# Optimization experiments

Measured on AMD Instinct MI355X. Metric: run time of the kernel, lower is better.

Reference implementation:

```python
import jax, jax.numpy as jnp
import numpy as np

WBITS = 4
ABITS = 8
OBITS = 8


def fwht(x):
    """Normalized fast Walsh-Hadamard transform along the last axis (n power of 2).
    Equivalent to matmul_hadU with had_K = I, K = 1 (n = 4096 = 2^12)."""
    shape = x.shape
    n = shape[-1]
    x = x.reshape(-1, n)
    h = 1
    while h < n:
        x = x.reshape(-1, n // (2 * h), 2, h)
        a, b = x[:, :, 0, :], x[:, :, 1, :]
        x = jnp.concatenate([a + b, a - b], axis=-1).reshape(-1, n)
        h *= 2
    inv_sqrt_n = jnp.asarray(1.0 / np.sqrt(n), x.dtype)
    return (x * inv_sqrt_n).reshape(shape)


def sym_fake_quant(t, bits, axis):
    """Symmetric min-max RTN fake quantization (per-channel for weights,
    per-token for activations)."""
    qmax = jnp.asarray(2.0 ** (bits - 1) - 1.0, t.dtype)
    scale = jnp.max(jnp.abs(t), axis=axis, keepdims=True) / qmax
    scale = jnp.maximum(scale, jnp.asarray(1e-8, t.dtype))
    q = jnp.clip(jnp.round(t / scale), -qmax, qmax)
    return q * scale


def setup_inputs() -> dict:
    key = jax.random.key(0)
    k1, k2, k3 = jax.random.split(key, 3)
    B, S, DIN, DOUT = 4, 2048, 4096, 4096
    return {
        "input": jax.random.normal(k1, (B, S, DIN), dtype=jnp.float32),
        "weight": jax.random.normal(k2, (DOUT, DIN), dtype=jnp.float32) * 0.02,
        "bias": jax.random.normal(k3, (DOUT,), dtype=jnp.float32) * 0.01,
    }


def reference(input, weight, bias):
    # online full Hadamard rotation of activations
    x = fwht(input)
    # activation quant (per-token, symmetric int8 fake-quant)
    x = sym_fake_quant(x, ABITS, axis=-1)
    # weight quant (per-output-channel, symmetric int4 fake-quant)
    w = sym_fake_quant(weight, WBITS, axis=-1)
    # F.linear: x @ w.T + b
    out = jnp.einsum("bsi,oi->bso", x, w) + bias
    # output quant (per-token, symmetric int8 fake-quant)
    out = sym_fake_quant(out, OBITS, axis=-1)
    return out
```

## Files before the change

### kernel.cpp

```cpp
#include <hip/hip_runtime.h>
#include <hip/hip_bf16.h>

#define DIN 4096
#define DOUT 4096
#define NROWS 8192

typedef int i32x4 __attribute__((ext_vector_type(4)));

__device__ __forceinline__ float block_absmax(float m, float* red) {
  #pragma unroll
  for (int off = 32; off > 0; off >>= 1)
    m = fmaxf(m, __shfl_down(m, off));
  const int tid = threadIdx.x;
  if ((tid & 63) == 0) red[tid >> 6] = m;
  __syncthreads();
  return fmaxf(fmaxf(red[0], red[1]), fmaxf(red[2], red[3]));
}

__global__ __launch_bounds__(256) void fwht_quant_kernel(
    const float* __restrict__ in, char* __restrict__ qx,
    float* __restrict__ sx) {
  __shared__ float lds[4352];
  __shared__ float red[4];
  const int tid = threadIdx.x;
  const size_t row = blockIdx.x;
  const int th = tid >> 4, tl = tid & 15;
  float v[16];

  const float4* src = (const float4*)(in + row * DIN);
  #pragma unroll
  for (int k = 0; k < 4; ++k) {
    float4 f = src[tid * 4 + k];
    v[4 * k + 0] = f.x; v[4 * k + 1] = f.y;
    v[4 * k + 2] = f.z; v[4 * k + 3] = f.w;
  }
  #pragma unroll
  for (int hb = 1; hb < 16; hb <<= 1)
    #pragma unroll
    for (int j = 0; j < 16; ++j)
      if (!(j & hb)) {
        float a0 = v[j], b0 = v[j | hb];
        v[j] = a0 + b0; v[j | hb] = a0 - b0;
      }
  #pragma unroll
  for (int j = 0; j < 16; ++j) lds[17 * tid + j] = v[j];
  __syncthreads();
  #pragma unroll
  for (int j = 0; j < 16; ++j) v[j] = lds[272 * th + 17 * j + tl];
  #pragma unroll
  for (int hb = 1; hb < 16; hb <<= 1)
    #pragma unroll
    for (int j = 0; j < 16; ++j)
      if (!(j & hb)) {
        float a0 = v[j], b0 = v[j | hb];
        v[j] = a0 + b0; v[j | hb] = a0 - b0;
      }
  #pragma unroll
  for (int j = 0; j < 16; ++j) lds[272 * th + 17 * j + tl] = v[j];
  __syncthreads();
  #pragma unroll
  for (int j = 0; j < 16; ++j) v[j] = lds[272 * j + 17 * th + tl];
  #pragma unroll
  for (int hb = 1; hb < 16; hb <<= 1)
    #pragma unroll
    for (int j = 0; j < 16; ++j)
      if (!(j & hb)) {
        float a0 = v[j], b0 = v[j | hb];
        v[j] = a0 + b0; v[j | hb] = a0 - b0;
      }
  float m = 0.0f;
  #pragma unroll
  for (int j = 0; j < 16; ++j) m = fmaxf(m, fabsf(v[j]));
  #pragma unroll
  for (int j = 0; j < 16; ++j) lds[272 * j + 17 * th + tl] = v[j];
  float mx = block_absmax(m, red) * 0.015625f;
  float scale = fmaxf(mx / 127.0f, 1e-8f);
  if (tid == 0) sx[row] = scale;
  const float rs = 1.0f / scale;
  char pk[16];
  #pragma unroll
  for (int j = 0; j < 16; ++j) {
    float q = fminf(fmaxf(rintf((lds[17 * tid + j] * 0.015625f) * rs), -127.f),
                    127.f);
    pk[j] = (char)q;
  }
  *(int4*)(qx + row * DIN + (size_t)tid * 16) = *(const int4*)pk;
}

__global__ __launch_bounds__(256) void wquant_kernel(
    const float* __restrict__ w, char* __restrict__ qw,
    float* __restrict__ sw) {
  __shared__ float buf[DIN];
  __shared__ float red[4];
  const int tid = threadIdx.x;
  const size_t row = blockIdx.x;
  const float4* src = (const float4*)(w + row * DIN);
  float4* b4 = (float4*)buf;
  float m = 0.0f;
  for (int i = tid; i < DIN / 4; i += 256) {
    float4 v = src[i];
    b4[i] = v;
    m = fmaxf(m, fmaxf(fmaxf(fabsf(v.x), fabsf(v.y)),
                       fmaxf(fabsf(v.z), fabsf(v.w))));
  }
  float mx = block_absmax(m, red);
  float scale = fmaxf(mx / 7.0f, 1e-8f);
  if (tid == 0) sw[row] = scale;
  char* dst = qw + row * DIN;
  const float rs = 1.0f / scale;
  for (int i0 = tid * 4; i0 < DIN; i0 += 1024) {
    char4 pk;
    float q0 = fminf(fmaxf(rintf(buf[i0 + 0] * rs), -7.f), 7.f);
    float q1 = fminf(fmaxf(rintf(buf[i0 + 1] * rs), -7.f), 7.f);
    float q2 = fminf(fmaxf(rintf(buf[i0 + 2] * rs), -7.f), 7.f);
    float q3 = fminf(fmaxf(rintf(buf[i0 + 3] * rs), -7.f), 7.f);
    pk.x = (char)q0; pk.y = (char)q1; pk.z = (char)q2; pk.w = (char)q3;
    *(char4*)(dst + i0) = pk;
  }
}

__global__ __launch_bounds__(512, 2) void gemm_kernel(
    const char* __restrict__ A,
    const char* __restrict__ Bt,
    const float* __restrict__ sx, const float* __restrict__ sw,
    const float* __restrict__ bias, float* __restrict__ out) {
  __shared__ char lds[131072];
  const int tid = threadIdx.x;
  const int lane = tid & 63;
  const int wid = tid >> 6;
  const int wr = wid >> 2;
  const int wc = wid & 3;
  int bid = blockIdx.x;
  int swz = (bid & 7) * 64 + (bid >> 3);
  const int tm = swz >> 4;
  const int tn = swz & 15;
  const size_t row0 = (size_t)tm * 256;
  const size_t col0 = (size_t)tn * 256;
  const int slot0 = (((lane >> 4) ^ (lane & 7)) << 4);

  i32x4 acc[4][2][4] = {};
  i32x4 fb[4][2];
  i32x4 fa[2][2];

#define STAGE(MAT, GROW0, KT, LBASE)                                          \
  {                                                                           \
    _Pragma("unroll")                                                         \
    for (int j = 0; j < 2; ++j) {                                             \
      int chunk = j * 8 + wid;                                                \
      int rr = chunk * 8 + (lane >> 3);                                       \
      int cc = (KT) * 128 + (((lane & 7) ^ (lane >> 3)) << 4);                \
      const char* src = (MAT) + ((GROW0) + rr) * (size_t)DIN + cc;            \
      __builtin_amdgcn_global_load_lds(                                       \
          (const __attribute__((address_space(1))) void*)src,                 \
          (__attribute__((address_space(3))) void*)(lds + (LBASE) +           \
                                                    chunk * 1024),            \
          16, 0, 0);                                                          \
    }                                                                         \
  }
#define STAGE_A(P, HALF, KT) \
  STAGE(A, row0 + (HALF) * 128, KT, (P) * 32768 + (HALF) * 16384)
#define STAGE_B(P, HALF, KT) \
  STAGE(Bt, col0 + (HALF) * 128, KT, 65536 + (P) * 32768 + (HALF) * 16384)

#define DS_A(Q, P)                                                            \
  {                                                                           \
    _Pragma("unroll")                                                         \
    for (int mm = 0; mm < 2; ++mm) {                                          \
      int ar = (Q) * 64 + wr * 32 + mm * 16 + (lane & 15);                    \
      _Pragma("unroll")                                                       \
      for (int kk = 0; kk < 2; ++kk)                                          \
        fa[mm][kk] =                                                          \
            *(const i32x4*)(lds + (P) * 32768 + ar * 128 + (slot0 ^ (kk * 64))); \
    }                                                                         \
  }
#define DS_B(P)                                                               \
  {                                                                           \
    _Pragma("unroll")                                                         \
    for (int nn = 0; nn < 4; ++nn) {                                          \
      int br = wc * 64 + nn * 16 + (lane & 15);                               \
      _Pragma("unroll")                                                       \
      for (int kk = 0; kk < 2; ++kk)                                          \
        fb[nn][kk] = *(const i32x4*)(lds + 65536 + (P) * 32768 + br * 128 +   \
                                     (slot0 ^ (kk * 64)));                    \
    }                                                                         \
  }
#define MFMA16(Q)                                                             \
  {                                                                           \
    __builtin_amdgcn_s_setprio(1);                                            \
    _Pragma("unroll")                                                         \
    for (int kk = 0; kk < 2; ++kk)                                            \
      _Pragma("unroll")                                                       \
      for (int mm = 0; mm < 2; ++mm)                                          \
        _Pragma("unroll")                                                     \
        for (int nn = 0; nn < 4; ++nn)                                        \
          acc[Q][mm][nn] = __builtin_amdgcn_mfma_i32_16x16x64_i8(             \
              fb[nn][kk], fa[mm][kk], acc[Q][mm][nn], 0, 0, 0);               \
    __builtin_amdgcn_s_setprio(0);                                            \
  }
#define BAR() __builtin_amdgcn_s_barrier()
#define WAIT_LGKM0() asm volatile("s_waitcnt lgkmcnt(0)" ::: "memory")

  STAGE_B(0, 0, 0); STAGE_B(0, 1, 0); STAGE_A(0, 0, 0); STAGE_A(0, 1, 0);
  STAGE_B(1, 0, 1); STAGE_B(1, 1, 1); STAGE_A(1, 0, 1);
  asm volatile("s_waitcnt vmcnt(6)" ::: "memory");
  BAR();

  #pragma unroll 1
  for (int i = 0; i < 16; ++i) {
    const int a = 2 * i, b = 2 * i + 1;
    const bool nl = (i < 15);
    DS_A(0, 0); DS_B(0);
    STAGE_A(1, 1, b);
    asm volatile("s_waitcnt lgkmcnt(8)" ::: "memory");
    BAR(); WAIT_LGKM0();
    MFMA16(0);
    BAR();
    DS_A(1, 0);
    if (nl) STAGE_B(0, 0, a + 2);
    BAR(); WAIT_LGKM0();
    MFMA16(1);
    BAR();
    DS_A(2, 0);
    if (nl) STAGE_B(0, 1, a + 2);
    BAR(); WAIT_LGKM0();
    MFMA16(2);
    BAR();
    DS_A(3, 0);
    if (nl) STAGE_A(0, 0, a + 2);
    BAR(); WAIT_LGKM0();
    MFMA16(3);
    if (nl) { asm volatile("s_waitcnt vmcnt(6)" ::: "memory"); }
    else    { asm volatile("s_waitcnt vmcnt(0)" ::: "memory"); }
    BAR();
    DS_A(0, 1); DS_B(1);
    if (nl) STAGE_A(0, 1, a + 2);
    asm volatile("s_waitcnt lgkmcnt(8)" ::: "memory");
    BAR(); WAIT_LGKM0();
    MFMA16(0);
    BAR();
    DS_A(1, 1);
    if (nl) STAGE_B(1, 0, b + 2);
    BAR(); WAIT_LGKM0();
    MFMA16(1);
    BAR();
    DS_A(2, 1);
    if (nl) STAGE_B(1, 1, b + 2);
    BAR(); WAIT_LGKM0();
    MFMA16(2);
    BAR();
    DS_A(3, 1);
    if (nl) STAGE_A(1, 0, b + 2);
    BAR(); WAIT_LGKM0();
    MFMA16(3);
    if (nl) { asm volatile("s_waitcnt vmcnt(6)" ::: "memory"); }
    BAR();
  }

  #pragma unroll
  for (int q = 0; q < 4; ++q) {
    #pragma unroll
    for (int mm = 0; mm < 2; ++mm) {
      size_t gr = row0 + q * 64 + wr * 32 + mm * 16 + (lane & 15);
      float sxr = sx[gr];
      float* orow = out + gr * DOUT;
      #pragma unroll
      for (int nn = 0; nn < 4; ++nn) {
        size_t gc0 = col0 + wc * 64 + nn * 16 + ((lane >> 4) << 2);
        float4 swv = *(const float4*)(sw + gc0);
        float4 bv = *(const float4*)(bias + gc0);
        float4 o;
        o.x = (float)acc[q][mm][nn][0] * (sxr * swv.x) + bv.x;
        o.y = (float)acc[q][mm][nn][1] * (sxr * swv.y) + bv.y;
        o.z = (float)acc[q][mm][nn][2] * (sxr * swv.z) + bv.z;
        o.w = (float)acc[q][mm][nn][3] * (sxr * swv.w) + bv.w;
        *(float4*)(orow + gc0) = o;
      }
    }
  }
#undef STAGE
#undef STAGE_A
#undef STAGE_B
#undef DS_A
#undef DS_B
#undef MFMA16
#undef BAR
#undef WAIT_LGKM0
}

__global__ __launch_bounds__(256) void rowquant_kernel(float* __restrict__ out) {
  __shared__ float red[4];
  const int tid = threadIdx.x;
  const size_t row = blockIdx.x;
  float4* g4 = (float4*)(out + row * DOUT);
  float4 v[4];
  float m = 0.0f;
  #pragma unroll
  for (int k = 0; k < 4; ++k) {
    v[k] = g4[tid + k * 256];
    m = fmaxf(m, fmaxf(fmaxf(fabsf(v[k].x), fabsf(v[k].y)),
                       fmaxf(fabsf(v[k].z), fabsf(v[k].w))));
  }
  float mx = block_absmax(m, red);
  float scale = fmaxf(mx / 127.0f, 1e-8f);
  #pragma unroll
  for (int k = 0; k < 4; ++k) {
    float4 w = v[k];
    w.x = fminf(fmaxf(rintf(w.x / scale), -127.0f), 127.0f) * scale;
    w.y = fminf(fmaxf(rintf(w.y / scale), -127.0f), 127.0f) * scale;
    w.z = fminf(fmaxf(rintf(w.z / scale), -127.0f), 127.0f) * scale;
    w.w = fminf(fmaxf(rintf(w.w / scale), -127.0f), 127.0f) * scale;
    g4[tid + k * 256] = w;
  }
}

extern "C" void kernel_launch(void* const* d_in, const int* in_sizes, int n_in,
                              void* d_out, int out_size, void* d_ws, size_t ws_size,
                              hipStream_t stream) {
  (void)in_sizes; (void)n_in; (void)out_size; (void)ws_size;
  const float* input = (const float*)d_in[0];
  const float* weight = (const float*)d_in[1];
  const float* bias = (const float*)d_in[2];
  float* out = (float*)d_out;
  char* ws = (char*)d_ws;
  char* qx = ws;
  char* qw = ws + ((size_t)32 << 20);
  float* sx = (float*)(ws + ((size_t)48 << 20));
  float* sw = (float*)(ws + ((size_t)48 << 20) + ((size_t)32 << 10));

  fwht_quant_kernel<<<NROWS, 256, 0, stream>>>(input, qx, sx);
  wquant_kernel<<<DOUT, 256, 0, stream>>>(weight, qw, sw);
  gemm_kernel<<<512, 512, 0, stream>>>(qx, qw, sx, sw, bias, out);
  rowquant_kernel<<<NROWS, 256, 0, stream>>>(out);
}
```

Baseline: 225.3 us.

## Switch int8 GEMM to 32x32x32 MFMA with double-buffered A fragments

Replaces the 16x16x64 int8 MFMA tiles with 32x32x32 int8 MFMAs and rewrites the LDS fragment loads and the epilogue mapping to match the new accumulator layout. A fragments are ping-ponged between two register sets so the next sub-tile's LDS reads overlap the current MFMA batch. Explicit lgkmcnt waits and extra barriers are replaced by sched_barrier hints, and vmcnt thresholds are retuned. The intent is to raise MFMA efficiency and cut LDS traffic and barrier stalls. The risks are correctness of the relaxed waits, where ordering of the LDS reads is left to the compiler, and higher register pressure from the double fragment buffers.

```diff
diff --git a/kernel.cpp b/kernel.cpp
--- a/kernel.cpp
+++ b/kernel.cpp
@@ -6,6 +6,7 @@
 #define NROWS 8192
 
 typedef int i32x4 __attribute__((ext_vector_type(4)));
+typedef int i32x16 __attribute__((ext_vector_type(16)));
 
 __device__ __forceinline__ float block_absmax(float m, float* red) {
   #pragma unroll
@@ -130,17 +131,16 @@
   const int wid = tid >> 6;
   const int wr = wid >> 2;
   const int wc = wid & 3;
+  const int lh = lane >> 5;
+  const int l31 = lane & 31;
   int bid = blockIdx.x;
   int swz = (bid & 7) * 64 + (bid >> 3);
-  const int tm = swz >> 4;
-  const int tn = swz & 15;
-  const size_t row0 = (size_t)tm * 256;
-  const size_t col0 = (size_t)tn * 256;
-  const int slot0 = (((lane >> 4) ^ (lane & 7)) << 4);
-
-  i32x4 acc[4][2][4] = {};
-  i32x4 fb[4][2];
-  i32x4 fa[2][2];
+  const size_t row0 = (size_t)(swz >> 4) * 256;
+  const size_t col0 = (size_t)(swz & 15) * 256;
+
+  i32x16 acc[4][2] = {};
+  i32x4 faA[4], faB[4];
+  i32x4 fb[2][4];
 
 #define STAGE(MAT, GROW0, KT, LBASE)                                          \
   {                                                                           \
@@ -162,117 +162,112 @@
 #define STAGE_B(P, HALF, KT) \
   STAGE(Bt, col0 + (HALF) * 128, KT, 65536 + (P) * 32768 + (HALF) * 16384)
 
-#define DS_A(Q, P)                                                            \
+#define DS_FA(DST, Q, P)                                                      \
+  {                                                                           \
+    int ar_ = (Q) * 64 + wr * 32 + l31;                                       \
+    _Pragma("unroll")                                                         \
+    for (int kk = 0; kk < 4; ++kk)                                            \
+      DST[kk] = *(const i32x4*)(lds + (P) * 32768 + ar_ * 128 +               \
+                                (((kk * 2 + lh) ^ (ar_ & 7)) << 4));          \
+  }
+#define DS_FB(P)                                                              \
   {                                                                           \
     _Pragma("unroll")                                                         \
-    for (int mm = 0; mm < 2; ++mm) {                                          \
-      int ar = (Q) * 64 + wr * 32 + mm * 16 + (lane & 15);                    \
+    for (int nn = 0; nn < 2; ++nn) {                                          \
+      int br_ = wc * 64 + nn * 32 + l31;                                      \
       _Pragma("unroll")                                                       \
-      for (int kk = 0; kk < 2; ++kk)                                          \
-        fa[mm][kk] =                                                          \
-            *(const i32x4*)(lds + (P) * 32768 + ar * 128 + (slot0 ^ (kk * 64))); \
+      for (int kk = 0; kk < 4; ++kk)                                          \
+        fb[nn][kk] = *(const i32x4*)(lds + 65536 + (P) * 32768 + br_ * 128 +  \
+                                     (((kk * 2 + lh) ^ (br_ & 7)) << 4));     \
     }                                                                         \
   }
-#define DS_B(P)                                                               \
-  {                                                                           \
-    _Pragma("unroll")                                                         \
-    for (int nn = 0; nn < 4; ++nn) {                                          \
-      int br = wc * 64 + nn * 16 + (lane & 15);                               \
-      _Pragma("unroll")                                                       \
-      for (int kk = 0; kk < 2; ++kk)                                          \
-        fb[nn][kk] = *(const i32x4*)(lds + 65536 + (P) * 32768 + br * 128 +   \
-                                     (slot0 ^ (kk * 64)));                    \
-    }                                                                         \
-  }
-#define MFMA16(Q)                                                             \
+#define MFMA8(Q, FA)                                                          \
   {                                                                           \
     __builtin_amdgcn_s_setprio(1);                                            \
     _Pragma("unroll")                                                         \
-    for (int kk = 0; kk < 2; ++kk)                                            \
+    for (int kk = 0; kk < 4; ++kk)                                            \
       _Pragma("unroll")                                                       \
-      for (int mm = 0; mm < 2; ++mm)                                          \
-        _Pragma("unroll")                                                     \
-        for (int nn = 0; nn < 4; ++nn)                                        \
-          acc[Q][mm][nn] = __builtin_amdgcn_mfma_i32_16x16x64_i8(             \
-              fb[nn][kk], fa[mm][kk], acc[Q][mm][nn], 0, 0, 0);               \
+      for (int nn = 0; nn < 2; ++nn)                                          \
+        acc[Q][nn] = __builtin_amdgcn_mfma_i32_32x32x32_i8(                   \
+            fb[nn][kk], FA[kk], acc[Q][nn], 0, 0, 0);                         \
     __builtin_amdgcn_s_setprio(0);                                            \
   }
 #define BAR() __builtin_amdgcn_s_barrier()
-#define WAIT_LGKM0() asm volatile("s_waitcnt lgkmcnt(0)" ::: "memory")
+#define SCHED0() __builtin_amdgcn_sched_barrier(0)
 
   STAGE_B(0, 0, 0); STAGE_B(0, 1, 0); STAGE_A(0, 0, 0); STAGE_A(0, 1, 0);
   STAGE_B(1, 0, 1); STAGE_B(1, 1, 1); STAGE_A(1, 0, 1);
   asm volatile("s_waitcnt vmcnt(6)" ::: "memory");
   BAR();
+  DS_FA(faA, 0, 0);
 
   #pragma unroll 1
   for (int i = 0; i < 16; ++i) {
     const int a = 2 * i, b = 2 * i + 1;
     const bool nl = (i < 15);
-    DS_A(0, 0); DS_B(0);
+    DS_FB(0);
+    DS_FA(faB, 1, 0);
     STAGE_A(1, 1, b);
-    asm volatile("s_waitcnt lgkmcnt(8)" ::: "memory");
-    BAR(); WAIT_LGKM0();
-    MFMA16(0);
-    BAR();
-    DS_A(1, 0);
+    SCHED0();
+    MFMA8(0, faA);
+    BAR();
+    DS_FA(faA, 2, 0);
     if (nl) STAGE_B(0, 0, a + 2);
-    BAR(); WAIT_LGKM0();
-    MFMA16(1);
-    BAR();
-    DS_A(2, 0);
+    SCHED0();
+    MFMA8(1, faB);
+    BAR();
+    DS_FA(faB, 3, 0);
     if (nl) STAGE_B(0, 1, a + 2);
-    BAR(); WAIT_LGKM0();
-    MFMA16(2);
-    BAR();
-    DS_A(3, 0);
+    SCHED0();
+    MFMA8(2, faA);
+    if (nl) { asm volatile("s_waitcnt vmcnt(4)" ::: "memory"); }
+    else    { asm volatile("s_waitcnt vmcnt(0)" ::: "memory"); }
+    BAR();
+    DS_FA(faA, 0, 1);
     if (nl) STAGE_A(0, 0, a + 2);
-    BAR(); WAIT_LGKM0();
-    MFMA16(3);
-    if (nl) { asm volatile("s_waitcnt vmcnt(6)" ::: "memory"); }
-    else    { asm volatile("s_waitcnt vmcnt(0)" ::: "memory"); }
-    BAR();
-    DS_A(0, 1); DS_B(1);
+    SCHED0();
+    MFMA8(3, faB);
+    BAR();
+    DS_FB(1);
+    DS_FA(faB, 1, 1);
     if (nl) STAGE_A(0, 1, a + 2);
-    asm volatile("s_waitcnt lgkmcnt(8)" ::: "memory");
-    BAR(); WAIT_LGKM0();
-    MFMA16(0);
-    BAR();
-    DS_A(1, 1);
+    SCHED0();
+    MFMA8(0, faA);
+    BAR();
+    DS_FA(faA, 2, 1);
     if (nl) STAGE_B(1, 0, b + 2);
-    BAR(); WAIT_LGKM0();
-    MFMA16(1);
-    BAR();
-    DS_A(2, 1);
+    SCHED0();
+    MFMA8(1, faB);
+    BAR();
+    DS_FA(faB, 3, 1);
     if (nl) STAGE_B(1, 1, b + 2);
-    BAR(); WAIT_LGKM0();
-    MFMA16(2);
-    BAR();
-    DS_A(3, 1);
-    if (nl) STAGE_A(1, 0, b + 2);
-    BAR(); WAIT_LGKM0();
-    MFMA16(3);
-    if (nl) { asm volatile("s_waitcnt vmcnt(6)" ::: "memory"); }
+    SCHED0();
+    MFMA8(2, faA);
+    if (nl) { asm volatile("s_waitcnt vmcnt(4)" ::: "memory"); }
+    BAR();
+    if (nl) { DS_FA(faA, 0, 0); STAGE_A(1, 0, b + 2); }
+    SCHED0();
+    MFMA8(3, faB);
     BAR();
   }
 
   #pragma unroll
   for (int q = 0; q < 4; ++q) {
+    size_t gr = row0 + q * 64 + wr * 32 + l31;
+    float sxr = sx[gr];
+    float* orow = out + gr * DOUT;
     #pragma unroll
-    for (int mm = 0; mm < 2; ++mm) {
-      size_t gr = row0 + q * 64 + wr * 32 + mm * 16 + (lane & 15);
-      float sxr = sx[gr];
-      float* orow = out + gr * DOUT;
+    for (int nn = 0; nn < 2; ++nn) {
       #pragma unroll
-      for (int nn = 0; nn < 4; ++nn) {
-        size_t gc0 = col0 + wc * 64 + nn * 16 + ((lane >> 4) << 2);
+      for (int r4 = 0; r4 < 4; ++r4) {
+        size_t gc0 = col0 + wc * 64 + nn * 32 + 8 * r4 + 4 * lh;
         float4 swv = *(const float4*)(sw + gc0);
         float4 bv = *(const float4*)(bias + gc0);
         float4 o;
-        o.x = (float)acc[q][mm][nn][0] * (sxr * swv.x) + bv.x;
-        o.y = (float)acc[q][mm][nn][1] * (sxr * swv.y) + bv.y;
-        o.z = (float)acc[q][mm][nn][2] * (sxr * swv.z) + bv.z;
-        o.w = (float)acc[q][mm][nn][3] * (sxr * swv.w) + bv.w;
+        o.x = (float)acc[q][nn][r4 * 4 + 0] * (sxr * swv.x) + bv.x;
+        o.y = (float)acc[q][nn][r4 * 4 + 1] * (sxr * swv.y) + bv.y;
+        o.z = (float)acc[q][nn][r4 * 4 + 2] * (sxr * swv.z) + bv.z;
+        o.w = (float)acc[q][nn][r4 * 4 + 3] * (sxr * swv.w) + bv.w;
         *(float4*)(orow + gc0) = o;
       }
     }
@@ -280,11 +275,11 @@
 #undef STAGE
 #undef STAGE_A
 #undef STAGE_B
-#undef DS_A
-#undef DS_B
-#undef MFMA16
+#undef DS_FA
+#undef DS_FB
+#undef MFMA8
 #undef BAR
-#undef WAIT_LGKM0
+#undef SCHED0
 }
 
 __global__ __launch_bounds__(256) void rowquant_kernel(float* __restrict__ out) {
```

Result: slower. 256.3 us (+13.8%).

## Merge activation and weight quant kernels; make GEMM persistent over two row tiles

Applied to the files above, without the earlier changes.

Activation FWHT-quant and weight quant are merged into a single launch, with block index selecting the role, which removes one launch and lets both run concurrently. The GEMM grid is halved to 256 blocks. Each block now computes two consecutive 256-row tiles for the same column tile, streaming K twice in one pipelined loop and writing the first tile's epilogue mid-loop. This removes the pipeline fill and drain between tiles and gives one block per CU on the 256-CU part, at the cost of a longer serial loop, a full vmcnt drain at the tile switch, and possible tail imbalance.

```diff
diff --git a/kernel.cpp b/kernel.cpp
--- a/kernel.cpp
+++ b/kernel.cpp
@@ -17,105 +17,101 @@
   return fmaxf(fmaxf(red[0], red[1]), fmaxf(red[2], red[3]));
 }
 
-__global__ __launch_bounds__(256) void fwht_quant_kernel(
-    const float* __restrict__ in, char* __restrict__ qx,
-    float* __restrict__ sx) {
+__global__ __launch_bounds__(256) void fused_quant_kernel(
+    const float* __restrict__ in, const float* __restrict__ w,
+    char* __restrict__ qx, char* __restrict__ qw,
+    float* __restrict__ sx, float* __restrict__ sw) {
   __shared__ float lds[4352];
   __shared__ float red[4];
   const int tid = threadIdx.x;
-  const size_t row = blockIdx.x;
-  const int th = tid >> 4, tl = tid & 15;
-  float v[16];
-
-  const float4* src = (const float4*)(in + row * DIN);
-  #pragma unroll
-  for (int k = 0; k < 4; ++k) {
-    float4 f = src[tid * 4 + k];
-    v[4 * k + 0] = f.x; v[4 * k + 1] = f.y;
-    v[4 * k + 2] = f.z; v[4 * k + 3] = f.w;
-  }
-  #pragma unroll
-  for (int hb = 1; hb < 16; hb <<= 1)
-    #pragma unroll
-    for (int j = 0; j < 16; ++j)
-      if (!(j & hb)) {
-        float a0 = v[j], b0 = v[j | hb];
-        v[j] = a0 + b0; v[j | hb] = a0 - b0;
-      }
-  #pragma unroll
-  for (int j = 0; j < 16; ++j) lds[17 * tid + j] = v[j];
-  __syncthreads();
-  #pragma unroll
-  for (int j = 0; j < 16; ++j) v[j] = lds[272 * th + 17 * j + tl];
-  #pragma unroll
-  for (int hb = 1; hb < 16; hb <<= 1)
-    #pragma unroll
-    for (int j = 0; j < 16; ++j)
-      if (!(j & hb)) {
-        float a0 = v[j], b0 = v[j | hb];
-        v[j] = a0 + b0; v[j | hb] = a0 - b0;
-      }
-  #pragma unroll
-  for (int j = 0; j < 16; ++j) lds[272 * th + 17 * j + tl] = v[j];
-  __syncthreads();
-  #pragma unroll
-  for (int j = 0; j < 16; ++j) v[j] = lds[272 * j + 17 * th + tl];
-  #pragma unroll
-  for (int hb = 1; hb < 16; hb <<= 1)
-    #pragma unroll
-    for (int j = 0; j < 16; ++j)
-      if (!(j & hb)) {
-        float a0 = v[j], b0 = v[j | hb];
-        v[j] = a0 + b0; v[j | hb] = a0 - b0;
-      }
-  float m = 0.0f;
-  #pragma unroll
-  for (int j = 0; j < 16; ++j) m = fmaxf(m, fabsf(v[j]));
-  #pragma unroll
-  for (int j = 0; j < 16; ++j) lds[272 * j + 17 * th + tl] = v[j];
-  float mx = block_absmax(m, red) * 0.015625f;
-  float scale = fmaxf(mx / 127.0f, 1e-8f);
-  if (tid == 0) sx[row] = scale;
-  const float rs = 1.0f / scale;
-  char pk[16];
-  #pragma unroll
-  for (int j = 0; j < 16; ++j) {
-    float q = fminf(fmaxf(rintf((lds[17 * tid + j] * 0.015625f) * rs), -127.f),
-                    127.f);
-    pk[j] = (char)q;
-  }
-  *(int4*)(qx + row * DIN + (size_t)tid * 16) = *(const int4*)pk;
-}
-
-__global__ __launch_bounds__(256) void wquant_kernel(
-    const float* __restrict__ w, char* __restrict__ qw,
-    float* __restrict__ sw) {
-  __shared__ float buf[DIN];
-  __shared__ float red[4];
-  const int tid = threadIdx.x;
-  const size_t row = blockIdx.x;
-  const float4* src = (const float4*)(w + row * DIN);
-  float4* b4 = (float4*)buf;
-  float m = 0.0f;
-  for (int i = tid; i < DIN / 4; i += 256) {
-    float4 v = src[i];
-    b4[i] = v;
-    m = fmaxf(m, fmaxf(fmaxf(fabsf(v.x), fabsf(v.y)),
-                       fmaxf(fabsf(v.z), fabsf(v.w))));
-  }
-  float mx = block_absmax(m, red);
-  float scale = fmaxf(mx / 7.0f, 1e-8f);
-  if (tid == 0) sw[row] = scale;
-  char* dst = qw + row * DIN;
-  const float rs = 1.0f / scale;
-  for (int i0 = tid * 4; i0 < DIN; i0 += 1024) {
-    char4 pk;
-    float q0 = fminf(fmaxf(rintf(buf[i0 + 0] * rs), -7.f), 7.f);
-    float q1 = fminf(fmaxf(rintf(buf[i0 + 1] * rs), -7.f), 7.f);
-    float q2 = fminf(fmaxf(rintf(buf[i0 + 2] * rs), -7.f), 7.f);
-    float q3 = fminf(fmaxf(rintf(buf[i0 + 3] * rs), -7.f), 7.f);
-    pk.x = (char)q0; pk.y = (char)q1; pk.z = (char)q2; pk.w = (char)q3;
-    *(char4*)(dst + i0) = pk;
+
+  if (blockIdx.x < NROWS) {
+    const size_t row = blockIdx.x;
+    const int th = tid >> 4, tl = tid & 15;
+    float v[16];
+    const float4* src = (const float4*)(in + row * DIN);
+    #pragma unroll
+    for (int k = 0; k < 4; ++k) {
+      float4 f = src[tid * 4 + k];
+      v[4 * k + 0] = f.x; v[4 * k + 1] = f.y;
+      v[4 * k + 2] = f.z; v[4 * k + 3] = f.w;
+    }
+    #pragma unroll
+    for (int hb = 1; hb < 16; hb <<= 1)
+      #pragma unroll
+      for (int j = 0; j < 16; ++j)
+        if (!(j & hb)) {
+          float a0 = v[j], b0 = v[j | hb];
+          v[j] = a0 + b0; v[j | hb] = a0 - b0;
+        }
+    #pragma unroll
+    for (int j = 0; j < 16; ++j) lds[17 * tid + j] = v[j];
+    __syncthreads();
+    #pragma unroll
+    for (int j = 0; j < 16; ++j) v[j] = lds[272 * th + 17 * j + tl];
+    #pragma unroll
+    for (int hb = 1; hb < 16; hb <<= 1)
+      #pragma unroll
+      for (int j = 0; j < 16; ++j)
+        if (!(j & hb)) {
+          float a0 = v[j], b0 = v[j | hb];
+          v[j] = a0 + b0; v[j | hb] = a0 - b0;
+        }
+    #pragma unroll
+    for (int j = 0; j < 16; ++j) lds[272 * th + 17 * j + tl] = v[j];
+    __syncthreads();
+    #pragma unroll
+    for (int j = 0; j < 16; ++j) v[j] = lds[272 * j + 17 * th + tl];
+    #pragma unroll
+    for (int hb = 1; hb < 16; hb <<= 1)
+      #pragma unroll
+      for (int j = 0; j < 16; ++j)
+        if (!(j & hb)) {
+          float a0 = v[j], b0 = v[j | hb];
+          v[j] = a0 + b0; v[j | hb] = a0 - b0;
+        }
+    float m = 0.0f;
+    #pragma unroll
+    for (int j = 0; j < 16; ++j) m = fmaxf(m, fabsf(v[j]));
+    #pragma unroll
+    for (int j = 0; j < 16; ++j) lds[272 * j + 17 * th + tl] = v[j];
+    float mx = block_absmax(m, red) * 0.015625f;
+    float scale = fmaxf(mx / 127.0f, 1e-8f);
+    if (tid == 0) sx[row] = scale;
+    const float rs = 1.0f / scale;
+    char pk[16];
+    #pragma unroll
+    for (int j = 0; j < 16; ++j) {
+      float q = fminf(fmaxf(rintf((lds[17 * tid + j] * 0.015625f) * rs), -127.f),
+                      127.f);
+      pk[j] = (char)q;
+    }
+    *(int4*)(qx + row * DIN + (size_t)tid * 16) = *(const int4*)pk;
+  } else {
+    const size_t row = blockIdx.x - NROWS;
+    const float4* src = (const float4*)(w + row * DIN);
+    float4* b4 = (float4*)lds;
+    float m = 0.0f;
+    for (int i = tid; i < DIN / 4; i += 256) {
+      float4 v = src[i];
+      b4[i] = v;
+      m = fmaxf(m, fmaxf(fmaxf(fabsf(v.x), fabsf(v.y)),
+                         fmaxf(fabsf(v.z), fabsf(v.w))));
+    }
+    float mx = block_absmax(m, red);
+    float scale = fmaxf(mx / 7.0f, 1e-8f);
+    if (tid == 0) sw[row] = scale;
+    char* dst = qw + row * DIN;
+    const float rs = 1.0f / scale;
+    for (int i0 = tid * 4; i0 < DIN; i0 += 1024) {
+      char4 pk;
+      float q0 = fminf(fmaxf(rintf(lds[i0 + 0] * rs), -7.f), 7.f);
+      float q1 = fminf(fmaxf(rintf(lds[i0 + 1] * rs), -7.f), 7.f);
+      float q2 = fminf(fmaxf(rintf(lds[i0 + 2] * rs), -7.f), 7.f);
+      float q3 = fminf(fmaxf(rintf(lds[i0 + 3] * rs), -7.f), 7.f);
+      pk.x = (char)q0; pk.y = (char)q1; pk.z = (char)q2; pk.w = (char)q3;
+      *(char4*)(dst + i0) = pk;
+    }
   }
 }
 
@@ -131,11 +127,9 @@
   const int wr = wid >> 2;
   const int wc = wid & 3;
   int bid = blockIdx.x;
-  int swz = (bid & 7) * 64 + (bid >> 3);
-  const int tm = swz >> 4;
-  const int tn = swz & 15;
-  const size_t row0 = (size_t)tm * 256;
-  const size_t col0 = (size_t)tn * 256;
+  int swz = (bid & 7) * 32 + (bid >> 3);
+  const size_t rowA = (size_t)(swz >> 4) * 512;
+  const size_t col0 = (size_t)(swz & 15) * 256;
   const int slot0 = (((lane >> 4) ^ (lane & 7)) << 4);
 
   i32x4 acc[4][2][4] = {};
@@ -148,7 +142,7 @@
     for (int j = 0; j < 2; ++j) {                                             \
       int chunk = j * 8 + wid;                                                \
       int rr = chunk * 8 + (lane >> 3);                                       \
-      int cc = (KT) * 128 + (((lane & 7) ^ (lane >> 3)) << 4);                \
+      int cc = ((KT) & 31) * 128 + (((lane & 7) ^ (lane >> 3)) << 4);         \
       const char* src = (MAT) + ((GROW0) + rr) * (size_t)DIN + cc;            \
       __builtin_amdgcn_global_load_lds(                                       \
           (const __attribute__((address_space(1))) void*)src,                 \
@@ -157,8 +151,9 @@
           16, 0, 0);                                                          \
     }                                                                         \
   }
-#define STAGE_A(P, HALF, KT) \
-  STAGE(A, row0 + (HALF) * 128, KT, (P) * 32768 + (HALF) * 16384)
+#define STAGE_A(P, HALF, KT)                                                  \
+  STAGE(A, rowA + (((KT) >= 32) ? 256 : 0) + (HALF) * 128, KT,                \
+        (P) * 32768 + (HALF) * 16384)
 #define STAGE_B(P, HALF, KT) \
   STAGE(Bt, col0 + (HALF) * 128, KT, 65536 + (P) * 32768 + (HALF) * 16384)
 
@@ -200,15 +195,51 @@
 #define BAR() __builtin_amdgcn_s_barrier()
 #define WAIT_LGKM0() asm volatile("s_waitcnt lgkmcnt(0)" ::: "memory")
 
+#define EPI(T)                                                                \
+  {                                                                           \
+    _Pragma("unroll")                                                         \
+    for (int q = 0; q < 4; ++q) {                                             \
+      _Pragma("unroll")                                                       \
+      for (int mm = 0; mm < 2; ++mm) {                                        \
+        size_t gr = rowA + (T) * 256 + q * 64 + wr * 32 + mm * 16 + (lane & 15); \
+        float sxr = sx[gr];                                                   \
+        float* orow = out + gr * DOUT;                                        \
+        _Pragma("unroll")                                                     \
+        for (int nn = 0; nn < 4; ++nn) {                                      \
+          size_t gc0 = col0 + wc * 64 + nn * 16 + ((lane >> 4) << 2);         \
+          float4 swv = *(const float4*)(sw + gc0);                            \
+          float4 bv = *(const float4*)(bias + gc0);                           \
+          float4 o;                                                           \
+          o.x = (float)acc[q][mm][nn][0] * (sxr * swv.x) + bv.x;              \
+          o.y = (float)acc[q][mm][nn][1] * (sxr * swv.y) + bv.y;              \
+          o.z = (float)acc[q][mm][nn][2] * (sxr * swv.z) + bv.z;              \
+          o.w = (float)acc[q][mm][nn][3] * (sxr * swv.w) + bv.w;              \
+          *(float4*)(orow + gc0) = o;                                         \
+        }                                                                     \
+      }                                                                       \
+    }                                                                         \
+  }
+
   STAGE_B(0, 0, 0); STAGE_B(0, 1, 0); STAGE_A(0, 0, 0); STAGE_A(0, 1, 0);
   STAGE_B(1, 0, 1); STAGE_B(1, 1, 1); STAGE_A(1, 0, 1);
   asm volatile("s_waitcnt vmcnt(6)" ::: "memory");
   BAR();
 
   #pragma unroll 1
-  for (int i = 0; i < 16; ++i) {
+  for (int i = 0; i < 32; ++i) {
     const int a = 2 * i, b = 2 * i + 1;
-    const bool nl = (i < 15);
+    const bool nl = (i < 31);
+    if (i == 16) {
+      EPI(0);
+      #pragma unroll
+      for (int q = 0; q < 4; ++q)
+        #pragma unroll
+        for (int mm = 0; mm < 2; ++mm)
+          #pragma unroll
+          for (int nn = 0; nn < 4; ++nn)
+            acc[q][mm][nn] = (i32x4){0, 0, 0, 0};
+      asm volatile("s_waitcnt vmcnt(0)" ::: "memory");
+    }
     DS_A(0, 0); DS_B(0);
     STAGE_A(1, 1, b);
     asm volatile("s_waitcnt lgkmcnt(8)" ::: "memory");
@@ -256,27 +287,7 @@
     BAR();
   }
 
-  #pragma unroll
-  for (int q = 0; q < 4; ++q) {
-    #pragma unroll
-    for (int mm = 0; mm < 2; ++mm) {
-      size_t gr = row0 + q * 64 + wr * 32 + mm * 16 + (lane & 15);
-      float sxr = sx[gr];
-      float* orow = out + gr * DOUT;
-      #pragma unroll
-      for (int nn = 0; nn < 4; ++nn) {
-        size_t gc0 = col0 + wc * 64 + nn * 16 + ((lane >> 4) << 2);
-        float4 swv = *(const float4*)(sw + gc0);
-        float4 bv = *(const float4*)(bias + gc0);
-        float4 o;
-        o.x = (float)acc[q][mm][nn][0] * (sxr * swv.x) + bv.x;
-        o.y = (float)acc[q][mm][nn][1] * (sxr * swv.y) + bv.y;
-        o.z = (float)acc[q][mm][nn][2] * (sxr * swv.z) + bv.z;
-        o.w = (float)acc[q][mm][nn][3] * (sxr * swv.w) + bv.w;
-        *(float4*)(orow + gc0) = o;
-      }
-    }
-  }
+  EPI(1);
 #undef STAGE
 #undef STAGE_A
 #undef STAGE_B
@@ -285,6 +296,7 @@
 #undef MFMA16
 #undef BAR
 #undef WAIT_LGKM0
+#undef EPI
 }
 
 __global__ __launch_bounds__(256) void rowquant_kernel(float* __restrict__ out) {
@@ -327,8 +339,8 @@
   float* sx = (float*)(ws + ((size_t)48 << 20));
   float* sw = (float*)(ws + ((size_t)48 << 20) + ((size_t)32 << 10));
 
-  fwht_quant_kernel<<<NROWS, 256, 0, stream>>>(input, qx, sx);
-  wquant_kernel<<<DOUT, 256, 0, stream>>>(weight, qw, sw);
-  gemm_kernel<<<512, 512, 0, stream>>>(qx, qw, sx, sw, bias, out);
+  fused_quant_kernel<<<NROWS + DOUT, 256, 0, stream>>>(input, weight, qx, qw,
+                                                       sx, sw);
+  gemm_kernel<<<256, 512, 0, stream>>>(qx, qw, sx, sw, bias, out);
   rowquant_kernel<<<NROWS, 256, 0, stream>>>(out);
 }
```

After: 229.5 us. Within noise of the previous version (+1.9%).
